# Performance work log

Measured on AMD Instinct MI355X. Metric: run time of the kernel, lower is better.

## Reference

```python
import jax, jax.numpy as jnp
import numpy as np

# 5-point Laplacian stencil (OIHW), scaled by 1/h^2 = N^2 at each level
FIXED = jnp.array([[[[0.0, 1.0, 0.0], [1.0, -4.0, 1.0], [0.0, 1.0, 0.0]]]], dtype=jnp.float32)
# flex_cycle schedule: depth-2 V-cycle, weighted Jacobi (smoother==1) everywhere
INTERGRID = [-1, -1, 0, 1, 1]
WEIGHT = [0.8, 0.8, 0.8, 0.8, 0.8]
N_GRID = 4096


def _conv(x, k, stride=1):
    return jax.lax.conv_general_dilated(x, k, (stride, stride), 'VALID',
                                        dimension_numbers=('NCHW', 'OIHW', 'NCHW'))


def _pad1(x):
    return jnp.pad(x, ((0, 0), (0, 0), (1, 1), (1, 1)))


def _apply_A(u):
    # F.conv2d(u, N^2 * stencil, padding=0) then zero-pad back to full size
    n = u.shape[-1]
    return _pad1(_conv(u, float(n * n) * FIXED))


def _jacobi(u, f, omega):
    # trainable_weight == 0 and trainable_stencil == fixed_stencil, so the
    # torch update collapses to standard weighted Jacobi
    n = u.shape[-1]
    central = -4.0 * float(n * n)
    return u + omega * (f - _apply_A(u)) / central


def _restrict(r, R):
    return _conv(r, R, stride=2)


def _prolong(u, P):
    up = jnp.repeat(jnp.repeat(u, 2, axis=2), 2, axis=3)  # nearest x2
    return _pad1(_conv(up, P))


def _vcycle(f, R, P):
    u = jnp.zeros_like(f)
    us, fs, lvl = [u], [f], 0
    for op, w in zip(INTERGRID, WEIGHT):
        if op == -1:  # smooth, restrict residual
            us[lvl] = _jacobi(us[lvl], fs[lvl], w)
            r = fs[lvl] - _apply_A(us[lvl])
            fs.append(_restrict(r, R))
            us.append(jnp.zeros_like(fs[-1]))
            lvl += 1
        elif op == 1:  # prolongate + correct, then smooth
            us[lvl - 1] = us[lvl - 1] + _prolong(us[lvl], P)
            lvl -= 1
            us[lvl] = _jacobi(us[lvl], fs[lvl], w)
        else:  # smooth in place
            us[lvl] = _jacobi(us[lvl], fs[lvl], w)
    return us[0]


def setup_inputs() -> dict:
    key = jax.random.key(0)
    f = jax.random.normal(key, (1, 1, N_GRID, N_GRID), dtype=jnp.float32)
    R = jnp.full((1, 1, 2, 2), 0.25, dtype=jnp.float32)
    P = jnp.array([[[[0.25, 0.5, 0.25], [0.5, 1.0, 0.5], [0.25, 0.5, 0.25]]]], dtype=jnp.float32)
    return {"f": f, "restriction_stencils": R, "prolongation_stencils": P}


def reference(f, restriction_stencils, prolongation_stencils):
    # forward() sets max_iter=1 and initial residual (u=0) is 1 > tol,
    # so exactly one flex_cycle runs
    u = _vcycle(f, restriction_stencils, prolongation_stencils)
    res = jnp.sum(jnp.abs(f - _apply_A(u))) / jnp.sum(jnp.abs(f))
    return (u, res)
```

## Files before the change

kernel.cpp:

```cpp
#include <hip/hip_runtime.h>

#define N0 4096
#define N1 2048
#define N2 1024

__global__ __launch_bounds__(256, 4) void k_res_restrict(const float* __restrict__ f,
                                                         float* __restrict__ fc,
                                                         int n, int nc) {
    const int tid = threadIdx.x;
    const int tx = tid & 63, ty = tid >> 6;
    const int fy0 = blockIdx.y * 16, fx0 = blockIdx.x * 256;
    const bool edge = (blockIdx.x == 0) | (blockIdx.y == 0) |
                      (blockIdx.x == gridDim.x - 1) | (blockIdx.y == gridDim.y - 1);

    float fa[6][6];
    if (!edge) {
        const float* fb = f + (size_t)(fy0 + 4 * ty - 1) * n + (fx0 + 4 * tx);
        #pragma unroll
        for (int rr = 0; rr < 6; ++rr) {
            const float* rp = fb + (size_t)rr * n;
            float4 o = *(const float4*)rp;
            fa[rr][0] = rp[-1];
            fa[rr][1] = o.x; fa[rr][2] = o.y; fa[rr][3] = o.z; fa[rr][4] = o.w;
            fa[rr][5] = rp[4];
        }
    } else {
        const bool laneL = (tx == 0), laneR = (tx == 63);
        #pragma unroll
        for (int rr = 0; rr < 6; ++rr) {
            int gy = max(0, min(n - 1, fy0 + 4 * ty - 1 + rr));
            const float* rowp = f + (size_t)gy * n;
            float4 o = *(const float4*)(rowp + fx0 + 4 * tx);
            float os = 0.f;
            if (laneL) os = rowp[max(0, fx0 - 1)];
            if (laneR) os = rowp[min(n - 1, fx0 + 256)];
            fa[rr][1] = o.x; fa[rr][2] = o.y; fa[rr][3] = o.z; fa[rr][4] = o.w;
            fa[rr][0] = __shfl_up(o.w, 1);
            fa[rr][5] = __shfl_down(o.x, 1);
            if (laneL) fa[rr][0] = os;
            if (laneR) fa[rr][5] = os;
        }
    }

    float rv[4][4];
    #pragma unroll
    for (int i = 0; i < 4; ++i) {
        #pragma unroll
        for (int j = 0; j < 4; ++j) {
            float c = fa[1 + i][1 + j];
            rv[i][j] = c + 0.2f * (fa[i][1 + j] + fa[2 + i][1 + j] +
                                   fa[1 + i][j] + fa[1 + i][2 + j] - 4.0f * c);
        }
    }
    if (edge) {
        #pragma unroll
        for (int i = 0; i < 4; ++i)
            #pragma unroll
            for (int j = 0; j < 4; ++j) {
                int gy = fy0 + 4 * ty + i, gx = fx0 + 4 * tx + j;
                if (gy == 0 || gy == n - 1 || gx == 0 || gx == n - 1)
                    rv[i][j] = fa[1 + i][1 + j];
            }
    }
    #pragma unroll
    for (int da = 0; da < 2; ++da) {
        float2 o;
        o.x = 0.25f * (rv[2*da][0] + rv[2*da][1] + rv[2*da+1][0] + rv[2*da+1][1]);
        o.y = 0.25f * (rv[2*da][2] + rv[2*da][3] + rv[2*da+1][2] + rv[2*da+1][3]);
        *(float2*)(fc + (size_t)(fy0 / 2 + 2 * ty + da) * nc + (fx0 / 2 + 2 * tx)) = o;
    }
}

template <bool RESID>
__global__ __launch_bounds__(512) void k_smooth_wide(
        const float* __restrict__ f, const float* __restrict__ uc,
        float* __restrict__ u, int n, int m, float cf, float cs,
        double* __restrict__ pT, double* __restrict__ pF) {
    __shared__ __align__(16) float su[RESID ? 18 : 1][260];
    __shared__ float sredT[8], sredF[8];
    const int tid = threadIdx.x;
    const int tx = tid & 63, ty = tid >> 6;
    const int bx0 = blockIdx.x * 256, by0 = blockIdx.y * 16;
    const int Y  = by0 + 2 * ty;
    const int A0 = by0 >> 1;
    const int A  = A0 + ty;
    const int C  = (bx0 >> 1) + 2 * tx;
    const bool laneL = (tx == 0), laneR = (tx == 63);
    const bool edge = (blockIdx.x == 0) | (blockIdx.y == 0) |
                      (blockIdx.x == gridDim.x - 1) | (blockIdx.y == gridDim.y - 1);

    float fr[4][6];
    float cu[3][4];
    float4 fH4 = make_float4(0.f, 0.f, 0.f, 0.f);
    float cH[4] = {0.f, 0.f, 0.f, 0.f};
    float fsd2[2] = {0.f, 0.f};
    float csd2[3] = {0.f, 0.f, 0.f};

    if (!edge) {
        const float* fb = f + (size_t)(Y - 1) * n + (bx0 + 4 * tx);
        #pragma unroll
        for (int r = 0; r < 4; ++r) {
            const float* rp = fb + (size_t)r * n;
            float4 o = *(const float4*)rp;
            fr[r][0] = rp[-1];
            fr[r][1] = o.x; fr[r][2] = o.y; fr[r][3] = o.z; fr[r][4] = o.w;
            fr[r][5] = rp[4];
        }
        const float* cb = uc + (size_t)(A - 1) * m + C;
        #pragma unroll
        for (int i = 0; i < 3; ++i) {
            const float* rp = cb + (size_t)i * m;
            float2 o = *(const float2*)rp;
            cu[i][0] = cs * rp[-1];
            cu[i][1] = cs * o.x; cu[i][2] = cs * o.y;
            cu[i][3] = cs * rp[2];
        }
        if (RESID) {
            if (ty == 0 || ty == 7) {
                const float* rp = f + (size_t)(ty == 0 ? by0 - 2 : by0 + 17) * n + (bx0 + 4 * tx);
                fH4 = *(const float4*)rp;
                const float* cp = uc + (size_t)(ty == 0 ? A0 - 2 : A0 + 9) * m + C;
                float2 oc = *(const float2*)cp;
                cH[0] = cs * cp[-1]; cH[1] = cs * oc.x; cH[2] = cs * oc.y; cH[3] = cs * cp[2];
            }
            if (laneL) {
                #pragma unroll
                for (int i = 0; i < 3; ++i) csd2[i] = uc[(size_t)(A - 1 + i) * m + (C - 2)];
                #pragma unroll
                for (int k = 0; k < 2; ++k) fsd2[k] = f[(size_t)(Y + k) * n + (bx0 - 2)];
            }
            if (laneR) {
                #pragma unroll
                for (int i = 0; i < 3; ++i) csd2[i] = uc[(size_t)(A - 1 + i) * m + (C + 3)];
                #pragma unroll
                for (int k = 0; k < 2; ++k) fsd2[k] = f[(size_t)(Y + k) * n + (bx0 + 257)];
            }
        }
    } else {
        #pragma unroll
        for (int r = 0; r < 4; ++r) {
            int gy = max(0, min(n - 1, Y - 1 + r));
            const float* rowp = f + (size_t)gy * n;
            float4 o = *(const float4*)(rowp + bx0 + 4 * tx);
            float fs = 0.f;
            if (laneL) fs = rowp[max(0, bx0 - 1)];
            if (laneR) fs = rowp[min(n - 1, bx0 + 256)];
            fr[r][1] = o.x; fr[r][2] = o.y; fr[r][3] = o.z; fr[r][4] = o.w;
            fr[r][0] = __shfl_up(o.w, 1);
            fr[r][5] = __shfl_down(o.x, 1);
            if (laneL) fr[r][0] = fs;
            if (laneR) fr[r][5] = fs;
        }
        #pragma unroll
        for (int i = 0; i < 3; ++i) {
            int ga = max(0, min(m - 1, A - 1 + i));
            const float* cp = uc + (size_t)ga * m;
            float2 o = *(const float2*)(cp + C);
            float csde = 0.f;
            if (laneL) csde = cp[max(0, C - 1)];
            if (laneR) csde = cp[min(m - 1, C + 2)];
            float l  = __shfl_up(o.y, 1);
            float rg = __shfl_down(o.x, 1);
            if (laneL) l  = csde;
            if (laneR) rg = csde;
            cu[i][0] = cs * l; cu[i][1] = cs * o.x; cu[i][2] = cs * o.y; cu[i][3] = cs * rg;
        }
        if (RESID) {
            if (ty == 0 || ty == 7) {
                const float* rowp = f + (size_t)max(0, min(n - 1, ty == 0 ? by0 - 2 : by0 + 17)) * n;
                fH4 = *(const float4*)(rowp + bx0 + 4 * tx);
                const float* cp = uc + (size_t)max(0, min(m - 1, ty == 0 ? A0 - 2 : A0 + 9)) * m;
                float2 oc = *(const float2*)(cp + C);
                float cHs = 0.f;
                if (laneL) cHs = cp[max(0, C - 1)];
                if (laneR) cHs = cp[min(m - 1, C + 2)];
                float l  = __shfl_up(oc.y, 1);
                float rg = __shfl_down(oc.x, 1);
                if (laneL) l  = cHs;
                if (laneR) rg = cHs;
                cH[0] = cs * l; cH[1] = cs * oc.x; cH[2] = cs * oc.y; cH[3] = cs * rg;
            }
            if (laneL) {
                #pragma unroll
                for (int i = 0; i < 3; ++i) {
                    int ga = max(0, min(m - 1, A - 1 + i));
                    csd2[i] = uc[(size_t)ga * m + max(0, C - 2)];
                }
                #pragma unroll
                for (int k = 0; k < 2; ++k)
                    fsd2[k] = f[(size_t)(Y + k) * n + max(0, bx0 - 2)];
            }
            if (laneR) {
                #pragma unroll
                for (int i = 0; i < 3; ++i) {
                    int ga = max(0, min(m - 1, A - 1 + i));
                    csd2[i] = uc[(size_t)ga * m + min(m - 1, C + 3)];
                }
                #pragma unroll
                for (int k = 0; k < 2; ++k)
                    fsd2[k] = f[(size_t)(Y + k) * n + min(n - 1, bx0 + 257)];
            }
        }
    }

    float h[3][6];
    #pragma unroll
    for (int i = 0; i < 3; ++i) {
        h[i][0] = 1.5f * cu[i][0] + 0.5f * cu[i][1];
        h[i][1] = 0.5f * cu[i][0] + 1.5f * cu[i][1];
        h[i][2] = 1.5f * cu[i][1] + 0.5f * cu[i][2];
        h[i][3] = 0.5f * cu[i][1] + 1.5f * cu[i][2];
        h[i][4] = 1.5f * cu[i][2] + 0.5f * cu[i][3];
        h[i][5] = 0.5f * cu[i][2] + 1.5f * cu[i][3];
    }
    float v[4][6];
    #pragma unroll
    for (int j = 0; j < 6; ++j) {
        v[0][j] = 1.5f * h[0][j] + 0.5f * h[1][j] + cf * fr[0][j];
        v[1][j] = 0.5f * h[0][j] + 1.5f * h[1][j] + cf * fr[1][j];
        v[2][j] = 1.5f * h[1][j] + 0.5f * h[2][j] + cf * fr[2][j];
        v[3][j] = 0.5f * h[1][j] + 1.5f * h[2][j] + cf * fr[3][j];
    }
    if (edge) {
        #pragma unroll
        for (int r = 0; r < 4; ++r)
            #pragma unroll
            for (int j = 0; j < 6; ++j) {
                int gy = Y - 1 + r, gx = bx0 + 4 * tx - 1 + j;
                if (gy == 0 || gy == n - 1 || gx == 0 || gx == n - 1) v[r][j] = cf * fr[r][j];
            }
    }
    float u2[2][4];
    #pragma unroll
    for (int rr = 0; rr < 2; ++rr)
        #pragma unroll
        for (int cc = 0; cc < 4; ++cc) {
            float vc = v[1 + rr][1 + cc];
            u2[rr][cc] = vc + cf * fr[1 + rr][1 + cc]
                       + 0.2f * (v[rr][1 + cc] + v[2 + rr][1 + cc] +
                                 v[1 + rr][cc] + v[1 + rr][2 + cc] - 4.0f * vc);
        }
    if (edge) {
        #pragma unroll
        for (int rr = 0; rr < 2; ++rr)
            #pragma unroll
            for (int cc = 0; cc < 4; ++cc) {
                int gy = Y + rr, gx = bx0 + 4 * tx + cc;
                if (gy == 0 || gy == n - 1 || gx == 0 || gx == n - 1)
                    u2[rr][cc] = v[1 + rr][1 + cc] + cf * fr[1 + rr][1 + cc];
            }
    }
    #pragma unroll
    for (int rr = 0; rr < 2; ++rr)
        *(float4*)(u + (size_t)(Y + rr) * n + (bx0 + 4 * tx)) =
            make_float4(u2[rr][0], u2[rr][1], u2[rr][2], u2[rr][3]);

    if (RESID) {
        if (ty == 0) {
            float hm[4] = { 0.5f * cH[0] + 1.5f * cH[1], 1.5f * cH[1] + 0.5f * cH[2],
                            0.5f * cH[1] + 1.5f * cH[2], 1.5f * cH[2] + 0.5f * cH[3] };
            float fmv[4] = { fH4.x, fH4.y, fH4.z, fH4.w };
            float vm[4], uHt[4];
            #pragma unroll
            for (int cc = 0; cc < 4; ++cc) vm[cc] = 0.5f * hm[cc] + 1.5f * h[0][1 + cc] + cf * fmv[cc];
            if (edge) {
                #pragma unroll
                for (int cc = 0; cc < 4; ++cc) {
                    int gx = bx0 + 4 * tx + cc;
                    if (gx == 0 || gx == n - 1) vm[cc] = cf * fmv[cc];
                }
            }
            #pragma unroll
            for (int cc = 0; cc < 4; ++cc) {
                float vc = v[0][1 + cc];
                uHt[cc] = vc + cf * fr[0][1 + cc]
                        + 0.2f * (vm[cc] + v[1][1 + cc] + v[0][cc] + v[0][2 + cc] - 4.0f * vc);
            }
            if (edge) {
                #pragma unroll
                for (int cc = 0; cc < 4; ++cc) {
                    int gx = bx0 + 4 * tx + cc;
                    if (gx == 0 || gx == n - 1) uHt[cc] = v[0][1 + cc] + cf * fr[0][1 + cc];
                }
            }
            *(float4*)&su[0][4 * tx] = make_float4(uHt[0], uHt[1], uHt[2], uHt[3]);
        }
        if (ty == 7) {
            float hp[4] = { 0.5f * cH[0] + 1.5f * cH[1], 1.5f * cH[1] + 0.5f * cH[2],
                            0.5f * cH[1] + 1.5f * cH[2], 1.5f * cH[2] + 0.5f * cH[3] };
            float fpv[4] = { fH4.x, fH4.y, fH4.z, fH4.w };
            float vp[4], uHb[4];
            #pragma unroll
            for (int cc = 0; cc < 4; ++cc) vp[cc] = 1.5f * h[2][1 + cc] + 0.5f * hp[cc] + cf * fpv[cc];
            if (edge) {
                #pragma unroll
                for (int cc = 0; cc < 4; ++cc) {
                    int gx = bx0 + 4 * tx + cc;
                    if (gx == 0 || gx == n - 1) vp[cc] = cf * fpv[cc];
                }
            }
            #pragma unroll
            for (int cc = 0; cc < 4; ++cc) {
                float vc = v[3][1 + cc];
                uHb[cc] = vc + cf * fr[3][1 + cc]
                        + 0.2f * (v[2][1 + cc] + vp[cc] + v[3][cc] + v[3][2 + cc] - 4.0f * vc);
            }
            if (edge) {
                #pragma unroll
                for (int cc = 0; cc < 4; ++cc) {
                    int gx = bx0 + 4 * tx + cc;
                    if (gx == 0 || gx == n - 1) uHb[cc] = v[3][1 + cc] + cf * fr[3][1 + cc];
                }
            }
            *(float4*)&su[17][4 * tx] = make_float4(uHb[0], uHb[1], uHb[2], uHb[3]);
        }
        float uL[2] = {0.f, 0.f}, uR[2] = {0.f, 0.f};
        if (laneL) {
            float hL[3];
            #pragma unroll
            for (int i = 0; i < 3; ++i) hL[i] = 0.5f * cs * csd2[i] + 1.5f * cu[i][0];
            float vL[2] = { 0.5f * hL[0] + 1.5f * hL[1] + cf * fsd2[0],
                            1.5f * hL[1] + 0.5f * hL[2] + cf * fsd2[1] };
            if (edge) {
                #pragma unroll
                for (int k = 0; k < 2; ++k) {
                    int gy = Y + k;
                    if (gy == 0 || gy == n - 1) vL[k] = cf * fsd2[k];
                }
            }
            #pragma unroll
            for (int rr = 0; rr < 2; ++rr) {
                float vc = v[1 + rr][0];
                uL[rr] = vc + cf * fr[1 + rr][0]
                       + 0.2f * (v[rr][0] + v[2 + rr][0] + vL[rr] + v[1 + rr][1] - 4.0f * vc);
                if (edge) {
                    int gy = Y + rr;
                    if (gy == 0 || gy == n - 1) uL[rr] = vc + cf * fr[1 + rr][0];
                }
            }
        }
        if (laneR) {
            float hR[3];
            #pragma unroll
            for (int i = 0; i < 3; ++i) hR[i] = 1.5f * cu[i][3] + 0.5f * cs * csd2[i];
            float vR[2] = { 0.5f * hR[0] + 1.5f * hR[1] + cf * fsd2[0],
                            1.5f * hR[1] + 0.5f * hR[2] + cf * fsd2[1] };
            if (edge) {
                #pragma unroll
                for (int k = 0; k < 2; ++k) {
                    int gy = Y + k;
                    if (gy == 0 || gy == n - 1) vR[k] = cf * fsd2[k];
                }
            }
            #pragma unroll
            for (int rr = 0; rr < 2; ++rr) {
                float vc = v[1 + rr][5];
                uR[rr] = vc + cf * fr[1 + rr][5]
                       + 0.2f * (v[rr][5] + v[2 + rr][5] + v[1 + rr][4] + vR[rr] - 4.0f * vc);
                if (edge) {
                    int gy = Y + rr;
                    if (gy == 0 || gy == n - 1) uR[rr] = vc + cf * fr[1 + rr][5];
                }
            }
        }
        #pragma unroll
        for (int rr = 0; rr < 2; ++rr)
            *(float4*)&su[2 * ty + 1 + rr][4 * tx] =
                make_float4(u2[rr][0], u2[rr][1], u2[rr][2], u2[rr][3]);
        __syncthreads();
        float4 tv = *(const float4*)&su[2 * ty][4 * tx];
        float4 bv = *(const float4*)&su[2 * ty + 3][4 * tx];
        float ta[4] = { tv.x, tv.y, tv.z, tv.w };
        float ba[4] = { bv.x, bv.y, bv.z, bv.w };
        float lft[2], rgt[2];
        lft[0] = __shfl_up(u2[0][3], 1);   lft[1] = __shfl_up(u2[1][3], 1);
        rgt[0] = __shfl_down(u2[0][0], 1); rgt[1] = __shfl_down(u2[1][0], 1);
        if (laneL) { lft[0] = uL[0]; lft[1] = uL[1]; }
        if (laneR) { rgt[0] = uR[0]; rgt[1] = uR[1]; }
        const float n2 = (float)n * (float)n;
        float accT = 0.0f, accF = 0.0f;
        #pragma unroll
        for (int rr = 0; rr < 2; ++rr)
            #pragma unroll
            for (int cc = 0; cc < 4; ++cc) {
                float up = (rr == 0) ? ta[cc] : u2[0][cc];
                float dn = (rr == 1) ? ba[cc] : u2[1][cc];
                float lf = (cc == 0) ? lft[rr] : u2[rr][cc - 1];
                float rt = (cc == 3) ? rgt[rr] : u2[rr][cc + 1];
                float uu = u2[rr][cc];
                float fij = fr[1 + rr][1 + cc];
                float L = up + dn + lf + rt - 4.0f * uu;
                float t = fabsf(fij - n2 * L);
                if (edge) {
                    int gy = Y + rr, gx = bx0 + 4 * tx + cc;
                    if (gy == 0 || gy == n - 1 || gx == 0 || gx == n - 1) t = fabsf(fij);
                }
                accT += t;
                accF += fabsf(fij);
            }
        #pragma unroll
        for (int off = 32; off > 0; off >>= 1) {
            accT += __shfl_down(accT, off);
            accF += __shfl_down(accF, off);
        }
        if (tx == 0) { sredT[ty] = accT; sredF[ty] = accF; }
        __syncthreads();
        if (tid == 0) {
            double sT = 0.0, sF = 0.0;
            #pragma unroll
            for (int w = 0; w < 8; ++w) { sT += (double)sredT[w]; sF += (double)sredF[w]; }
            int bid = blockIdx.y * gridDim.x + blockIdx.x;
            pT[bid] = sT;
            pF[bid] = sF;
        }
    }
}

__global__ void k_final(const double* __restrict__ pT, const double* __restrict__ pF,
                        int nb, float* __restrict__ out_res) {
    __shared__ double sT[256], sF[256];
    double tT = 0.0, tF = 0.0;
    for (int i = threadIdx.x; i < nb; i += 256) { tT += pT[i]; tF += pF[i]; }
    sT[threadIdx.x] = tT; sF[threadIdx.x] = tF;
    __syncthreads();
    for (int s = 128; s > 0; s >>= 1) {
        if (threadIdx.x < s) { sT[threadIdx.x] += sT[threadIdx.x + s]; sF[threadIdx.x] += sF[threadIdx.x + s]; }
        __syncthreads();
    }
    if (threadIdx.x == 0) *out_res = (float)(sT[0] / sF[0]);
}

extern "C" void kernel_launch(void* const* d_in, const int* in_sizes, int n_in,
                              void* d_out, int out_size, void* d_ws, size_t ws_size,
                              hipStream_t stream) {
    const float* f0 = (const float*)d_in[0];
    float* u0  = (float*)d_out;
    float* res = u0 + (size_t)N0 * N0;

    char* ws = (char*)d_ws;
    float* f1 = (float*)ws;
    float* u1 = (float*)(ws + (size_t)N1 * N1 * 4);
    float* f2 = (float*)(ws + (size_t)2 * N1 * N1 * 4);
    double* pT = (double*)(ws + (size_t)2 * N1 * N1 * 4 + (size_t)N2 * N2 * 4);
    const int NB = (N0 / 256) * (N0 / 16);
    double* pF = pT + NB;

    const float c0 = -0.2f / ((float)N0 * (float)N0);
    const float c1 = -0.2f / ((float)N1 * (float)N1);
    const float c2 = -0.2f / ((float)N2 * (float)N2);

    k_res_restrict<<<dim3(N0 / 256, N0 / 16), 256, 0, stream>>>(f0, f1, N0, N1);
    k_res_restrict<<<dim3(N1 / 256, N1 / 16), 256, 0, stream>>>(f1, f2, N1, N2);
    k_smooth_wide<false><<<dim3(N1 / 256, N1 / 16), 512, 0, stream>>>(
        f1, f2, u1, N1, N2, c1, c2, nullptr, nullptr);
    k_smooth_wide<true><<<dim3(N0 / 256, N0 / 16), 512, 0, stream>>>(
        f0, u1, u0, N0, N1, c0, 1.0f, pT, pF);
    k_final<<<1, 256, 0, stream>>>(pT, pF, NB, res);
}
```

Measured before the change: 91.25 us.

## Compute four fine rows per thread in smooth kernel and unify restrict loads

The fused prolong-smooth-residual kernel now computes four output rows per thread (32-row block tiles) instead of two. This cuts the redundant halo loads of f and coarse u, and the coarse-row interpolation work shared between neighbouring rows. The grid and partial-sum count shrink to match, and launch bounds add an occupancy hint. In exchange, register pressure rises with larger per-thread arrays. The restrict kernel drops its separate interior path and always uses clamped loads plus lane shuffles, which trades two scalar halo loads per row for shuffles and clamp arithmetic.

Measured after the change: 98.10 us. 7.5% more time.

```diff
diff --git a/kernel.cpp b/kernel.cpp
--- a/kernel.cpp
+++ b/kernel.cpp
@@ -10,38 +10,28 @@
     const int tid = threadIdx.x;
     const int tx = tid & 63, ty = tid >> 6;
     const int fy0 = blockIdx.y * 16, fx0 = blockIdx.x * 256;
+    const bool laneL = (tx == 0), laneR = (tx == 63);
     const bool edge = (blockIdx.x == 0) | (blockIdx.y == 0) |
                       (blockIdx.x == gridDim.x - 1) | (blockIdx.y == gridDim.y - 1);
 
+    float4 o4[6]; float os[6];
+    #pragma unroll
+    for (int rr = 0; rr < 6; ++rr) {
+        int gy = max(0, min(n - 1, fy0 + 4 * ty - 1 + rr));
+        const float* rowp = f + (size_t)gy * n;
+        o4[rr] = *(const float4*)(rowp + fx0 + 4 * tx);
+        if (laneL) os[rr] = rowp[max(0, fx0 - 1)];
+        if (laneR) os[rr] = rowp[min(n - 1, fx0 + 256)];
+    }
     float fa[6][6];
-    if (!edge) {
-        const float* fb = f + (size_t)(fy0 + 4 * ty - 1) * n + (fx0 + 4 * tx);
-        #pragma unroll
-        for (int rr = 0; rr < 6; ++rr) {
-            const float* rp = fb + (size_t)rr * n;
-            float4 o = *(const float4*)rp;
-            fa[rr][0] = rp[-1];
-            fa[rr][1] = o.x; fa[rr][2] = o.y; fa[rr][3] = o.z; fa[rr][4] = o.w;
-            fa[rr][5] = rp[4];
-        }
-    } else {
-        const bool laneL = (tx == 0), laneR = (tx == 63);
-        #pragma unroll
-        for (int rr = 0; rr < 6; ++rr) {
-            int gy = max(0, min(n - 1, fy0 + 4 * ty - 1 + rr));
-            const float* rowp = f + (size_t)gy * n;
-            float4 o = *(const float4*)(rowp + fx0 + 4 * tx);
-            float os = 0.f;
-            if (laneL) os = rowp[max(0, fx0 - 1)];
-            if (laneR) os = rowp[min(n - 1, fx0 + 256)];
-            fa[rr][1] = o.x; fa[rr][2] = o.y; fa[rr][3] = o.z; fa[rr][4] = o.w;
-            fa[rr][0] = __shfl_up(o.w, 1);
-            fa[rr][5] = __shfl_down(o.x, 1);
-            if (laneL) fa[rr][0] = os;
-            if (laneR) fa[rr][5] = os;
-        }
-    }
-
+    #pragma unroll
+    for (int rr = 0; rr < 6; ++rr) {
+        fa[rr][1] = o4[rr].x; fa[rr][2] = o4[rr].y; fa[rr][3] = o4[rr].z; fa[rr][4] = o4[rr].w;
+        fa[rr][0] = __shfl_up(o4[rr].w, 1);
+        fa[rr][5] = __shfl_down(o4[rr].x, 1);
+        if (laneL) fa[rr][0] = os[rr];
+        if (laneR) fa[rr][5] = os[rr];
+    }
     float rv[4][4];
     #pragma unroll
     for (int i = 0; i < 4; ++i) {
@@ -72,34 +62,34 @@
 }
 
 template <bool RESID>
-__global__ __launch_bounds__(512) void k_smooth_wide(
+__global__ __launch_bounds__(512, 3) void k_smooth_wide(
         const float* __restrict__ f, const float* __restrict__ uc,
         float* __restrict__ u, int n, int m, float cf, float cs,
         double* __restrict__ pT, double* __restrict__ pF) {
-    __shared__ __align__(16) float su[RESID ? 18 : 1][260];
+    __shared__ __align__(16) float su[RESID ? 34 : 1][260];
     __shared__ float sredT[8], sredF[8];
     const int tid = threadIdx.x;
     const int tx = tid & 63, ty = tid >> 6;
-    const int bx0 = blockIdx.x * 256, by0 = blockIdx.y * 16;
-    const int Y  = by0 + 2 * ty;
+    const int bx0 = blockIdx.x * 256, by0 = blockIdx.y * 32;
+    const int Y  = by0 + 4 * ty;
     const int A0 = by0 >> 1;
-    const int A  = A0 + ty;
+    const int A  = A0 + 2 * ty;
     const int C  = (bx0 >> 1) + 2 * tx;
     const bool laneL = (tx == 0), laneR = (tx == 63);
     const bool edge = (blockIdx.x == 0) | (blockIdx.y == 0) |
                       (blockIdx.x == gridDim.x - 1) | (blockIdx.y == gridDim.y - 1);
 
-    float fr[4][6];
-    float cu[3][4];
+    float fr[6][6];
+    float cu[4][4];
     float4 fH4 = make_float4(0.f, 0.f, 0.f, 0.f);
     float cH[4] = {0.f, 0.f, 0.f, 0.f};
-    float fsd2[2] = {0.f, 0.f};
-    float csd2[3] = {0.f, 0.f, 0.f};
+    float fsd[4] = {0.f, 0.f, 0.f, 0.f};
+    float csd2[4] = {0.f, 0.f, 0.f, 0.f};
 
     if (!edge) {
         const float* fb = f + (size_t)(Y - 1) * n + (bx0 + 4 * tx);
         #pragma unroll
-        for (int r = 0; r < 4; ++r) {
+        for (int r = 0; r < 6; ++r) {
             const float* rp = fb + (size_t)r * n;
             float4 o = *(const float4*)rp;
             fr[r][0] = rp[-1];
@@ -108,7 +98,7 @@
         }
         const float* cb = uc + (size_t)(A - 1) * m + C;
         #pragma unroll
-        for (int i = 0; i < 3; ++i) {
+        for (int i = 0; i < 4; ++i) {
             const float* rp = cb + (size_t)i * m;
             float2 o = *(const float2*)rp;
             cu[i][0] = cs * rp[-1];
@@ -117,28 +107,28 @@
         }
         if (RESID) {
             if (ty == 0 || ty == 7) {
-                const float* rp = f + (size_t)(ty == 0 ? by0 - 2 : by0 + 17) * n + (bx0 + 4 * tx);
+                const float* rp = f + (size_t)(ty == 0 ? by0 - 2 : by0 + 33) * n + (bx0 + 4 * tx);
                 fH4 = *(const float4*)rp;
-                const float* cp = uc + (size_t)(ty == 0 ? A0 - 2 : A0 + 9) * m + C;
+                const float* cp = uc + (size_t)(ty == 0 ? A0 - 2 : A0 + 17) * m + C;
                 float2 oc = *(const float2*)cp;
                 cH[0] = cs * cp[-1]; cH[1] = cs * oc.x; cH[2] = cs * oc.y; cH[3] = cs * cp[2];
             }
             if (laneL) {
                 #pragma unroll
-                for (int i = 0; i < 3; ++i) csd2[i] = uc[(size_t)(A - 1 + i) * m + (C - 2)];
-                #pragma unroll
-                for (int k = 0; k < 2; ++k) fsd2[k] = f[(size_t)(Y + k) * n + (bx0 - 2)];
+                for (int i = 0; i < 4; ++i) csd2[i] = uc[(size_t)(A - 1 + i) * m + (C - 2)];
+                #pragma unroll
+                for (int k = 0; k < 4; ++k) fsd[k] = f[(size_t)(Y + k) * n + (bx0 - 2)];
             }
             if (laneR) {
                 #pragma unroll
-                for (int i = 0; i < 3; ++i) csd2[i] = uc[(size_t)(A - 1 + i) * m + (C + 3)];
-                #pragma unroll
-                for (int k = 0; k < 2; ++k) fsd2[k] = f[(size_t)(Y + k) * n + (bx0 + 257)];
+                for (int i = 0; i < 4; ++i) csd2[i] = uc[(size_t)(A - 1 + i) * m + (C + 3)];
+                #pragma unroll
+                for (int k = 0; k < 4; ++k) fsd[k] = f[(size_t)(Y + k) * n + (bx0 + 257)];
             }
         }
     } else {
         #pragma unroll
-        for (int r = 0; r < 4; ++r) {
+        for (int r = 0; r < 6; ++r) {
             int gy = max(0, min(n - 1, Y - 1 + r));
             const float* rowp = f + (size_t)gy * n;
             float4 o = *(const float4*)(rowp + bx0 + 4 * tx);
@@ -152,7 +142,7 @@
             if (laneR) fr[r][5] = fs;
         }
         #pragma unroll
-        for (int i = 0; i < 3; ++i) {
+        for (int i = 0; i < 4; ++i) {
             int ga = max(0, min(m - 1, A - 1 + i));
             const float* cp = uc + (size_t)ga * m;
             float2 o = *(const float2*)(cp + C);
@@ -167,9 +157,9 @@
         }
         if (RESID) {
             if (ty == 0 || ty == 7) {
-                const float* rowp = f + (size_t)max(0, min(n - 1, ty == 0 ? by0 - 2 : by0 + 17)) * n;
+                const float* rowp = f + (size_t)max(0, min(n - 1, ty == 0 ? by0 - 2 : by0 + 33)) * n;
                 fH4 = *(const float4*)(rowp + bx0 + 4 * tx);
-                const float* cp = uc + (size_t)max(0, min(m - 1, ty == 0 ? A0 - 2 : A0 + 9)) * m;
+                const float* cp = uc + (size_t)max(0, min(m - 1, ty == 0 ? A0 - 2 : A0 + 17)) * m;
                 float2 oc = *(const float2*)(cp + C);
                 float cHs = 0.f;
                 if (laneL) cHs = cp[max(0, C - 1)];
@@ -182,30 +172,30 @@
             }
             if (laneL) {
                 #pragma unroll
-                for (int i = 0; i < 3; ++i) {
+                for (int i = 0; i < 4; ++i) {
                     int ga = max(0, min(m - 1, A - 1 + i));
                     csd2[i] = uc[(size_t)ga * m + max(0, C - 2)];
                 }
                 #pragma unroll
-                for (int k = 0; k < 2; ++k)
-                    fsd2[k] = f[(size_t)(Y + k) * n + max(0, bx0 - 2)];
+                for (int k = 0; k < 4; ++k)
+                    fsd[k] = f[(size_t)max(0, min(n - 1, Y + k)) * n + max(0, bx0 - 2)];
             }
             if (laneR) {
                 #pragma unroll
-                for (int i = 0; i < 3; ++i) {
+                for (int i = 0; i < 4; ++i) {
                     int ga = max(0, min(m - 1, A - 1 + i));
                     csd2[i] = uc[(size_t)ga * m + min(m - 1, C + 3)];
                 }
                 #pragma unroll
-                for (int k = 0; k < 2; ++k)
-                    fsd2[k] = f[(size_t)(Y + k) * n + min(n - 1, bx0 + 257)];
-            }
-        }
-    }
-
-    float h[3][6];
-    #pragma unroll
-    for (int i = 0; i < 3; ++i) {
+                for (int k = 0; k < 4; ++k)
+                    fsd[k] = f[(size_t)max(0, min(n - 1, Y + k)) * n + min(n - 1, bx0 + 257)];
+            }
+        }
+    }
+
+    float h[4][6];
+    #pragma unroll
+    for (int i = 0; i < 4; ++i) {
         h[i][0] = 1.5f * cu[i][0] + 0.5f * cu[i][1];
         h[i][1] = 0.5f * cu[i][0] + 1.5f * cu[i][1];
         h[i][2] = 1.5f * cu[i][1] + 0.5f * cu[i][2];
@@ -213,47 +203,49 @@
         h[i][4] = 1.5f * cu[i][2] + 0.5f * cu[i][3];
         h[i][5] = 0.5f * cu[i][2] + 1.5f * cu[i][3];
     }
-    float v[4][6];
+    float v[6][6];
     #pragma unroll
     for (int j = 0; j < 6; ++j) {
         v[0][j] = 1.5f * h[0][j] + 0.5f * h[1][j] + cf * fr[0][j];
         v[1][j] = 0.5f * h[0][j] + 1.5f * h[1][j] + cf * fr[1][j];
         v[2][j] = 1.5f * h[1][j] + 0.5f * h[2][j] + cf * fr[2][j];
         v[3][j] = 0.5f * h[1][j] + 1.5f * h[2][j] + cf * fr[3][j];
+        v[4][j] = 1.5f * h[2][j] + 0.5f * h[3][j] + cf * fr[4][j];
+        v[5][j] = 0.5f * h[2][j] + 1.5f * h[3][j] + cf * fr[5][j];
     }
     if (edge) {
         #pragma unroll
-        for (int r = 0; r < 4; ++r)
+        for (int r = 0; r < 6; ++r)
             #pragma unroll
             for (int j = 0; j < 6; ++j) {
                 int gy = Y - 1 + r, gx = bx0 + 4 * tx - 1 + j;
                 if (gy == 0 || gy == n - 1 || gx == 0 || gx == n - 1) v[r][j] = cf * fr[r][j];
             }
     }
-    float u2[2][4];
-    #pragma unroll
-    for (int rr = 0; rr < 2; ++rr)
+    float u2[4][4];
+    #pragma unroll
+    for (int k = 0; k < 4; ++k)
         #pragma unroll
         for (int cc = 0; cc < 4; ++cc) {
-            float vc = v[1 + rr][1 + cc];
-            u2[rr][cc] = vc + cf * fr[1 + rr][1 + cc]
-                       + 0.2f * (v[rr][1 + cc] + v[2 + rr][1 + cc] +
-                                 v[1 + rr][cc] + v[1 + rr][2 + cc] - 4.0f * vc);
+            float vc = v[1 + k][1 + cc];
+            u2[k][cc] = vc + cf * fr[1 + k][1 + cc]
+                      + 0.2f * (v[k][1 + cc] + v[2 + k][1 + cc] +
+                                v[1 + k][cc] + v[1 + k][2 + cc] - 4.0f * vc);
         }
     if (edge) {
         #pragma unroll
-        for (int rr = 0; rr < 2; ++rr)
+        for (int k = 0; k < 4; ++k)
             #pragma unroll
             for (int cc = 0; cc < 4; ++cc) {
-                int gy = Y + rr, gx = bx0 + 4 * tx + cc;
+                int gy = Y + k, gx = bx0 + 4 * tx + cc;
                 if (gy == 0 || gy == n - 1 || gx == 0 || gx == n - 1)
-                    u2[rr][cc] = v[1 + rr][1 + cc] + cf * fr[1 + rr][1 + cc];
-            }
-    }
-    #pragma unroll
-    for (int rr = 0; rr < 2; ++rr)
-        *(float4*)(u + (size_t)(Y + rr) * n + (bx0 + 4 * tx)) =
-            make_float4(u2[rr][0], u2[rr][1], u2[rr][2], u2[rr][3]);
+                    u2[k][cc] = v[1 + k][1 + cc] + cf * fr[1 + k][1 + cc];
+            }
+    }
+    #pragma unroll
+    for (int k = 0; k < 4; ++k)
+        *(float4*)(u + (size_t)(Y + k) * n + (bx0 + 4 * tx)) =
+            make_float4(u2[k][0], u2[k][1], u2[k][2], u2[k][3]);
 
     if (RESID) {
         if (ty == 0) {
@@ -291,7 +283,7 @@
             float fpv[4] = { fH4.x, fH4.y, fH4.z, fH4.w };
             float vp[4], uHb[4];
             #pragma unroll
-            for (int cc = 0; cc < 4; ++cc) vp[cc] = 1.5f * h[2][1 + cc] + 0.5f * hp[cc] + cf * fpv[cc];
+            for (int cc = 0; cc < 4; ++cc) vp[cc] = 1.5f * h[3][1 + cc] + 0.5f * hp[cc] + cf * fpv[cc];
             if (edge) {
                 #pragma unroll
                 for (int cc = 0; cc < 4; ++cc) {
@@ -301,98 +293,109 @@
             }
             #pragma unroll
             for (int cc = 0; cc < 4; ++cc) {
-                float vc = v[3][1 + cc];
-                uHb[cc] = vc + cf * fr[3][1 + cc]
-                        + 0.2f * (v[2][1 + cc] + vp[cc] + v[3][cc] + v[3][2 + cc] - 4.0f * vc);
+                float vc = v[5][1 + cc];
+                uHb[cc] = vc + cf * fr[5][1 + cc]
+                        + 0.2f * (v[4][1 + cc] + vp[cc] + v[5][cc] + v[5][2 + cc] - 4.0f * vc);
             }
             if (edge) {
                 #pragma unroll
                 for (int cc = 0; cc < 4; ++cc) {
                     int gx = bx0 + 4 * tx + cc;
-                    if (gx == 0 || gx == n - 1) uHb[cc] = v[3][1 + cc] + cf * fr[3][1 + cc];
-                }
-            }
-            *(float4*)&su[17][4 * tx] = make_float4(uHb[0], uHb[1], uHb[2], uHb[3]);
-        }
-        float uL[2] = {0.f, 0.f}, uR[2] = {0.f, 0.f};
+                    if (gx == 0 || gx == n - 1) uHb[cc] = v[5][1 + cc] + cf * fr[5][1 + cc];
+                }
+            }
+            *(float4*)&su[33][4 * tx] = make_float4(uHb[0], uHb[1], uHb[2], uHb[3]);
+        }
+        float uL[4] = {0.f, 0.f, 0.f, 0.f}, uR[4] = {0.f, 0.f, 0.f, 0.f};
         if (laneL) {
-            float hL[3];
-            #pragma unroll
-            for (int i = 0; i < 3; ++i) hL[i] = 0.5f * cs * csd2[i] + 1.5f * cu[i][0];
-            float vL[2] = { 0.5f * hL[0] + 1.5f * hL[1] + cf * fsd2[0],
-                            1.5f * hL[1] + 0.5f * hL[2] + cf * fsd2[1] };
-            if (edge) {
-                #pragma unroll
-                for (int k = 0; k < 2; ++k) {
+            float hL[4];
+            #pragma unroll
+            for (int i = 0; i < 4; ++i) hL[i] = 0.5f * cs * csd2[i] + 1.5f * cu[i][0];
+            float vL[4] = { 0.5f * hL[0] + 1.5f * hL[1] + cf * fsd[0],
+                            1.5f * hL[1] + 0.5f * hL[2] + cf * fsd[1],
+                            0.5f * hL[1] + 1.5f * hL[2] + cf * fsd[2],
+                            1.5f * hL[2] + 0.5f * hL[3] + cf * fsd[3] };
+            if (edge) {
+                #pragma unroll
+                for (int k = 0; k < 4; ++k) {
                     int gy = Y + k;
-                    if (gy == 0 || gy == n - 1) vL[k] = cf * fsd2[k];
-                }
-            }
-            #pragma unroll
-            for (int rr = 0; rr < 2; ++rr) {
-                float vc = v[1 + rr][0];
-                uL[rr] = vc + cf * fr[1 + rr][0]
-                       + 0.2f * (v[rr][0] + v[2 + rr][0] + vL[rr] + v[1 + rr][1] - 4.0f * vc);
+                    if (gy == 0 || gy == n - 1) vL[k] = cf * fsd[k];
+                }
+            }
+            #pragma unroll
+            for (int k = 0; k < 4; ++k) {
+                float vc = v[1 + k][0];
+                uL[k] = vc + cf * fr[1 + k][0]
+                      + 0.2f * (v[k][0] + v[2 + k][0] + vL[k] + v[1 + k][1] - 4.0f * vc);
                 if (edge) {
-                    int gy = Y + rr;
-                    if (gy == 0 || gy == n - 1) uL[rr] = vc + cf * fr[1 + rr][0];
+                    int gy = Y + k;
+                    if (gy == 0 || gy == n - 1) uL[k] = vc + cf * fr[1 + k][0];
                 }
             }
         }
         if (laneR) {
-            float hR[3];
-            #pragma unroll
-            for (int i = 0; i < 3; ++i) hR[i] = 1.5f * cu[i][3] + 0.5f * cs * csd2[i];
-            float vR[2] = { 0.5f * hR[0] + 1.5f * hR[1] + cf * fsd2[0],
-                            1.5f * hR[1] + 0.5f * hR[2] + cf * fsd2[1] };
-            if (edge) {
-                #pragma unroll
-                for (int k = 0; k < 2; ++k) {
+            float hR[4];
+            #pragma unroll
+            for (int i = 0; i < 4; ++i) hR[i] = 1.5f * cu[i][3] + 0.5f * cs * csd2[i];
+            float vR[4] = { 0.5f * hR[0] + 1.5f * hR[1] + cf * fsd[0],
+                            1.5f * hR[1] + 0.5f * hR[2] + cf * fsd[1],
+                            0.5f * hR[1] + 1.5f * hR[2] + cf * fsd[2],
+                            1.5f * hR[2] + 0.5f * hR[3] + cf * fsd[3] };
+            if (edge) {
+                #pragma unroll
+                for (int k = 0; k < 4; ++k) {
                     int gy = Y + k;
-                    if (gy == 0 || gy == n - 1) vR[k] = cf * fsd2[k];
-                }
-            }
-            #pragma unroll
-            for (int rr = 0; rr < 2; ++rr) {
-                float vc = v[1 + rr][5];
-                uR[rr] = vc + cf * fr[1 + rr][5]
-                       + 0.2f * (v[rr][5] + v[2 + rr][5] + v[1 + rr][4] + vR[rr] - 4.0f * vc);
+                    if (gy == 0 || gy == n - 1) vR[k] = cf * fsd[k];
+                }
+            }
+            #pragma unroll
+            for (int k = 0; k < 4; ++k) {
+                float vc = v[1 + k][5];
+                uR[k] = vc + cf * fr[1 + k][5]
+                      + 0.2f * (v[k][5] + v[2 + k][5] + v[1 + k][4] + vR[k] - 4.0f * vc);
                 if (edge) {
-                    int gy = Y + rr;
-                    if (gy == 0 || gy == n - 1) uR[rr] = vc + cf * fr[1 + rr][5];
-                }
-            }
-        }
-        #pragma unroll
-        for (int rr = 0; rr < 2; ++rr)
-            *(float4*)&su[2 * ty + 1 + rr][4 * tx] =
-                make_float4(u2[rr][0], u2[rr][1], u2[rr][2], u2[rr][3]);
+                    int gy = Y + k;
+                    if (gy == 0 || gy == n - 1) uR[k] = vc + cf * fr[1 + k][5];
+                }
+            }
+        }
+        #pragma unroll
+        for (int k = 0; k < 4; ++k)
+            *(float4*)&su[4 * ty + 1 + k][4 * tx] =
+                make_float4(u2[k][0], u2[k][1], u2[k][2], u2[k][3]);
         __syncthreads();
-        float4 tv = *(const float4*)&su[2 * ty][4 * tx];
-        float4 bv = *(const float4*)&su[2 * ty + 3][4 * tx];
+        float4 tv = *(const float4*)&su[4 * ty][4 * tx];
+        float4 bv = *(const float4*)&su[4 * ty + 5][4 * tx];
         float ta[4] = { tv.x, tv.y, tv.z, tv.w };
         float ba[4] = { bv.x, bv.y, bv.z, bv.w };
-        float lft[2], rgt[2];
-        lft[0] = __shfl_up(u2[0][3], 1);   lft[1] = __shfl_up(u2[1][3], 1);
-        rgt[0] = __shfl_down(u2[0][0], 1); rgt[1] = __shfl_down(u2[1][0], 1);
-        if (laneL) { lft[0] = uL[0]; lft[1] = uL[1]; }
-        if (laneR) { rgt[0] = uR[0]; rgt[1] = uR[1]; }
+        float lft[4], rgt[4];
+        #pragma unroll
+        for (int k = 0; k < 4; ++k) {
+            lft[k] = __shfl_up(u2[k][3], 1);
+            rgt[k] = __shfl_down(u2[k][0], 1);
+        }
+        if (laneL) {
+            for (int k = 0; k < 4; ++k) lft[k] = uL[k];
+        }
+        if (laneR) {
+            for (int k = 0; k < 4; ++k) rgt[k] = uR[k];
+        }
         const float n2 = (float)n * (float)n;
         float accT = 0.0f, accF = 0.0f;
         #pragma unroll
-        for (int rr = 0; rr < 2; ++rr)
+        for (int k = 0; k < 4; ++k)
             #pragma unroll
             for (int cc = 0; cc < 4; ++cc) {
-                float up = (rr == 0) ? ta[cc] : u2[0][cc];
-                float dn = (rr == 1) ? ba[cc] : u2[1][cc];
-                float lf = (cc == 0) ? lft[rr] : u2[rr][cc - 1];
-                float rt = (cc == 3) ? rgt[rr] : u2[rr][cc + 1];
-                float uu = u2[rr][cc];
-                float fij = fr[1 + rr][1 + cc];
+                float up = (k == 0) ? ta[cc] : u2[k - 1][cc];
+                float dn = (k == 3) ? ba[cc] : u2[k + 1][cc];
+                float lf = (cc == 0) ? lft[k] : u2[k][cc - 1];
+                float rt = (cc == 3) ? rgt[k] : u2[k][cc + 1];
+                float uu = u2[k][cc];
+                float fij = fr[1 + k][1 + cc];
                 float L = up + dn + lf + rt - 4.0f * uu;
                 float t = fabsf(fij - n2 * L);
                 if (edge) {
-                    int gy = Y + rr, gx = bx0 + 4 * tx + cc;
+                    int gy = Y + k, gx = bx0 + 4 * tx + cc;
                     if (gy == 0 || gy == n - 1 || gx == 0 || gx == n - 1) t = fabsf(fij);
                 }
                 accT += t;
@@ -442,7 +445,7 @@
     float* u1 = (float*)(ws + (size_t)N1 * N1 * 4);
     float* f2 = (float*)(ws + (size_t)2 * N1 * N1 * 4);
     double* pT = (double*)(ws + (size_t)2 * N1 * N1 * 4 + (size_t)N2 * N2 * 4);
-    const int NB = (N0 / 256) * (N0 / 16);
+    const int NB = (N0 / 256) * (N0 / 32);
     double* pF = pT + NB;
 
     const float c0 = -0.2f / ((float)N0 * (float)N0);
@@ -451,9 +454,9 @@
 
     k_res_restrict<<<dim3(N0 / 256, N0 / 16), 256, 0, stream>>>(f0, f1, N0, N1);
     k_res_restrict<<<dim3(N1 / 256, N1 / 16), 256, 0, stream>>>(f1, f2, N1, N2);
-    k_smooth_wide<false><<<dim3(N1 / 256, N1 / 16), 512, 0, stream>>>(
+    k_smooth_wide<false><<<dim3(N1 / 256, N1 / 32), 512, 0, stream>>>(
         f1, f2, u1, N1, N2, c1, c2, nullptr, nullptr);
-    k_smooth_wide<true><<<dim3(N0 / 256, N0 / 16), 512, 0, stream>>>(
+    k_smooth_wide<true><<<dim3(N0 / 256, N0 / 32), 512, 0, stream>>>(
         f0, u1, u0, N0, N1, c0, 1.0f, pT, pF);
     k_final<<<1, 256, 0, stream>>>(pT, pF, NB, res);
 }
```
